# Kernel tuning notes

Hardware: AMD Instinct MI355X
Metric: run time of the kernel (lower is better)

Reference implementation:

```python
import jax, jax.numpy as jnp
import numpy as np

# dims: B batch, R seq_num (MSA rows), L seq_len (residues), D emb_dim, C n_emb_2D, H heads
B, R, L, D, C, H = 1, 256, 384, 512, 256, 4
HD = D // H
SCALE = np.float32((HD ** -0.5) / np.sqrt(L))  # head-dim scaling * seqlen_scaling (1/sqrt(L))
EPS = 1e-5


def setup_inputs() -> dict:
    key = jax.random.key(0)
    ks = jax.random.split(key, 6)
    s = 0.02
    return {
        "x": jax.random.normal(ks[0], (B, R, L, D), jnp.float32),
        "pair_feat": jax.random.normal(ks[1], (B, L, L, C), jnp.float32),
        "attn_mask": jnp.ones((B, L), jnp.int32),
        "ln_msa_g": jnp.ones((D,), jnp.float32),
        "ln_msa_b": jnp.zeros((D,), jnp.float32),
        "ln_pair_g": jnp.ones((C,), jnp.float32),
        "ln_pair_b": jnp.zeros((C,), jnp.float32),
        "W_pair": jax.random.normal(ks[2], (C, H), jnp.float32) * s,  # stacked per-head [C,1] linears
        "W_v": jax.random.normal(ks[3], (D, D), jnp.float32) * s,     # stacked per-head [D,HD] value proj
        "W_out": jax.random.normal(ks[4], (D, D), jnp.float32) * s,   # to_out (bias=False)
    }


def _ln(x, g, b):
    mu = jnp.mean(x, axis=-1, keepdims=True)
    var = jnp.mean(jnp.square(x - mu), axis=-1, keepdims=True)
    return (x - mu) * jax.lax.rsqrt(var + EPS) * g + b


def reference(x, pair_feat, attn_mask, ln_msa_g, ln_msa_b, ln_pair_g, ln_pair_b, W_pair, W_v, W_out):
    # MHPair_to_MSA.forward (eval mode, dropout=0)
    msa = _ln(x, ln_msa_g, ln_msa_b)                                  # [B,R,L,D]
    pf = (pair_feat + jnp.swapaxes(pair_feat, 1, 2)) * 0.5            # symmetrize
    pf = _ln(pf, ln_pair_g, ln_pair_b)                                # [B,L,L,C]
    # pair-feature-derived attention logits (no QK^T)
    logits = jnp.einsum('bijc,ch->bhij', pf * SCALE, W_pair)          # [B,H,L,L]
    V = jnp.einsum('brld,de->brle', msa, W_v).reshape(B, R, L, H, HD) # [B,R,L,H,HD]
    mask2 = attn_mask[:, :, None] * attn_mask[:, None, :]             # [B,L,L]
    logits = jnp.where(mask2[:, None, :, :] == 0,
                       jnp.finfo(logits.dtype).min, logits)
    attn = jax.nn.softmax(logits, axis=-1)                            # [B,H,L,L]
    out = jnp.einsum('bhij,brjhd->brihd', attn, V).reshape(B, R, L, D)
    out = out @ W_out                                                 # to_out, bias=False
    return x + out                                                    # residual
```

## Files before the change

kernel.cpp:

```cpp
#include <hip/hip_runtime.h>

#define L_   384
#define D_   512
#define C_   256
#define H_   4
#define RR_  256
#define M1_  98304
#define LL2_ 147456
#define NPAIR_BLOCKS 18480
#define TILE_ELEMS (128 * 64)

typedef __bf16 bf16x8 __attribute__((ext_vector_type(8)));
typedef float f32x4 __attribute__((ext_vector_type(4)));

__device__ __forceinline__ unsigned short f2bf_bits(float f) {
  union { float f; unsigned u; } v; v.f = f;
  return (unsigned short)((v.u + 0x7fffu + ((v.u >> 16) & 1u)) >> 16);
}
__device__ __forceinline__ __bf16 f2bf(float f) {
  union { unsigned short s; __bf16 b; } o; o.s = f2bf_bits(f);
  return o.b;
}

__device__ __forceinline__ float wave_sum(float v) {
#pragma unroll
  for (int o = 32; o > 0; o >>= 1) v += __shfl_xor(v, o);
  return v;
}
__device__ __forceinline__ float wave_max(float v) {
#pragma unroll
  for (int o = 32; o > 0; o >>= 1) v = fmaxf(v, __shfl_xor(v, o));
  return v;
}

__global__ __launch_bounds__(256) void ln_msa_kernel(
    const float* __restrict__ x, const float* __restrict__ g,
    const float* __restrict__ b, __bf16* __restrict__ msa) {
  int row = blockIdx.x * 4 + (threadIdx.x >> 6);
  int lane = threadIdx.x & 63;
  const float4* xr = (const float4*)(x + (size_t)row * D_ + lane * 8);
  float4 v0 = xr[0], v1 = xr[1];
  float s1 = v0.x + v0.y + v0.z + v0.w + v1.x + v1.y + v1.z + v1.w;
  float s2 = v0.x * v0.x + v0.y * v0.y + v0.z * v0.z + v0.w * v0.w +
             v1.x * v1.x + v1.y * v1.y + v1.z * v1.z + v1.w * v1.w;
#pragma unroll
  for (int o = 32; o > 0; o >>= 1) {
    s1 += __shfl_xor(s1, o);
    s2 += __shfl_xor(s2, o);
  }
  float mu = s1 * (1.0f / D_);
  float var = s2 * (1.0f / D_) - mu * mu;
  float rs = rsqrtf(var + 1e-5f);
  const float4* gp = (const float4*)(g + lane * 8);
  const float4* bp = (const float4*)(b + lane * 8);
  float4 g0 = gp[0], g1 = gp[1], b0 = bp[0], b1 = bp[1];
  float y[8];
  y[0] = (v0.x - mu) * rs * g0.x + b0.x;
  y[1] = (v0.y - mu) * rs * g0.y + b0.y;
  y[2] = (v0.z - mu) * rs * g0.z + b0.z;
  y[3] = (v0.w - mu) * rs * g0.w + b0.w;
  y[4] = (v1.x - mu) * rs * g1.x + b1.x;
  y[5] = (v1.y - mu) * rs * g1.y + b1.y;
  y[6] = (v1.z - mu) * rs * g1.z + b1.z;
  y[7] = (v1.w - mu) * rs * g1.w + b1.w;
  uint4 pk;
  pk.x = ((unsigned)f2bf_bits(y[1]) << 16) | f2bf_bits(y[0]);
  pk.y = ((unsigned)f2bf_bits(y[3]) << 16) | f2bf_bits(y[2]);
  pk.z = ((unsigned)f2bf_bits(y[5]) << 16) | f2bf_bits(y[4]);
  pk.w = ((unsigned)f2bf_bits(y[7]) << 16) | f2bf_bits(y[6]);
  *(uint4*)(msa + (size_t)row * D_ + lane * 8) = pk;
}

__global__ __launch_bounds__(256) void pair_logits_kernel(
    const float* __restrict__ pf, const int* __restrict__ mask,
    const float* __restrict__ g, const float* __restrict__ b,
    const float* __restrict__ Wp, float* __restrict__ logits) {
  unsigned wid = blockIdx.x * 4 + (threadIdx.x >> 6);
  int lane = threadIdx.x & 63;
  unsigned a = wid / 385u;
  unsigned c = wid - a * 385u;
  int i, j;
  if (c < 384u - a) { i = a; j = a + c; }
  else { i = 383 - a; j = i + (c - (384 - a)); }

  int c0 = lane * 4;
  float4 p1 = *(const float4*)(pf + ((size_t)i * L_ + j) * C_ + c0);
  float4 p2 = *(const float4*)(pf + ((size_t)j * L_ + i) * C_ + c0);
  float4 v;
  v.x = 0.5f * (p1.x + p2.x); v.y = 0.5f * (p1.y + p2.y);
  v.z = 0.5f * (p1.z + p2.z); v.w = 0.5f * (p1.w + p2.w);
  float s1 = v.x + v.y + v.z + v.w;
  float s2 = v.x * v.x + v.y * v.y + v.z * v.z + v.w * v.w;
#pragma unroll
  for (int o = 32; o > 0; o >>= 1) {
    s1 += __shfl_xor(s1, o);
    s2 += __shfl_xor(s2, o);
  }
  float mu = s1 * (1.0f / C_);
  float var = s2 * (1.0f / C_) - mu * mu;
  float rs = rsqrtf(var + 1e-5f);
  float4 gv = *(const float4*)(g + c0);
  float4 bv = *(const float4*)(b + c0);
  float y0 = (v.x - mu) * rs * gv.x + bv.x;
  float y1 = (v.y - mu) * rs * gv.y + bv.y;
  float y2 = (v.z - mu) * rs * gv.z + bv.z;
  float y3 = (v.w - mu) * rs * gv.w + bv.w;
  const float4* wp = (const float4*)Wp;
  float4 w0 = wp[c0], w1 = wp[c0 + 1], w2 = wp[c0 + 2], w3 = wp[c0 + 3];
  float4 t;
  t.x = y0 * w0.x + y1 * w1.x + y2 * w2.x + y3 * w3.x;
  t.y = y0 * w0.y + y1 * w1.y + y2 * w2.y + y3 * w3.y;
  t.z = y0 * w0.z + y1 * w1.z + y2 * w2.z + y3 * w3.z;
  t.w = y0 * w0.w + y1 * w1.w + y2 * w2.w + y3 * w3.w;
#pragma unroll
  for (int o = 32; o > 0; o >>= 1) {
    t.x += __shfl_xor(t.x, o);
    t.y += __shfl_xor(t.y, o);
    t.z += __shfl_xor(t.z, o);
    t.w += __shfl_xor(t.w, o);
  }
  if (lane < 8) {
    int h = lane & 3;
    int ii = (lane < 4) ? i : j;
    int jj = (lane < 4) ? j : i;
    bool ok = (mask[i] != 0) && (mask[j] != 0);
    const float NEG = -3.402823466e38f;
    const float SCALE = (float)(0.08838834764831845 / 19.595917942265423);
    float th = (h == 0) ? t.x : (h == 1) ? t.y : (h == 2) ? t.z : t.w;
    logits[(size_t)h * LL2_ + (size_t)ii * L_ + jj] = ok ? SCALE * th : NEG;
  }
}

__global__ __launch_bounds__(256) void softmax_kernel(
    const float* __restrict__ logits, __bf16* __restrict__ attn) {
  int wave = threadIdx.x >> 6, lane = threadIdx.x & 63;
  int row = blockIdx.x * 4 + wave;
  const float* lr = logits + (size_t)row * L_;
  float v[6];
#pragma unroll
  for (int t = 0; t < 6; ++t) v[t] = lr[lane + t * 64];
  float mx = v[0];
#pragma unroll
  for (int t = 1; t < 6; ++t) mx = fmaxf(mx, v[t]);
  mx = wave_max(mx);
  float s = 0.f;
#pragma unroll
  for (int t = 0; t < 6; ++t) { v[t] = __expf(v[t] - mx); s += v[t]; }
  s = wave_sum(s);
  float inv = 1.0f / s;
  __bf16* ar = attn + (size_t)row * L_;
#pragma unroll
  for (int t = 0; t < 6; ++t) ar[lane + t * 64] = f2bf(v[t] * inv);
}

__global__ __launch_bounds__(256) void wtrans_kernel(
    const float* __restrict__ Wv, const float* __restrict__ Wo,
    __bf16* __restrict__ WvT, __bf16* __restrict__ WoT) {
  int id = blockIdx.x * 256 + threadIdx.x;
  int m = id >> 18;
  int e = (id >> 9) & 511, d = id & 511;
  const float* W = m ? Wo : Wv;
  __bf16* T = m ? WoT : WvT;
  T[(size_t)e * 512 + d] = f2bf(W[(size_t)d * 512 + e]);
}

__device__ __forceinline__ void gload16(const void* g, void* l) {
  __builtin_amdgcn_global_load_lds(
      (const __attribute__((address_space(1))) void*)g,
      (__attribute__((address_space(3))) void*)l, 16, 0, 0);
}

__device__ __forceinline__ void stage_tile_async(__bf16* s, const __bf16* g, size_t ld) {
  int tid = threadIdx.x;
#pragma unroll
  for (int it = 0; it < 4; ++it) {
    int cid = it * 256 + tid;
    int row = cid >> 3, chk = cid & 7;
    int src_off = (chk * 16) ^ ((row & 7) << 4);
    gload16(g + (size_t)row * ld + (src_off >> 1), (char*)s + cid * 16);
  }
}

__device__ __forceinline__ bf16x8 frag_ld(const __bf16* s, int row, int k) {
  int sb = row * 128 + ((k * 2) ^ ((row & 7) << 4));
  return *(const bf16x8*)((const char*)s + sb);
}

__device__ __forceinline__ void gemm_mainloop(
    const __bf16* __restrict__ Arow, size_t ldA,
    const __bf16* __restrict__ Brow, size_t ldB,
    int K, __bf16* As, __bf16* Bs, f32x4 acc[4][4]) {
  int lane = threadIdx.x & 63, wave = threadIdx.x >> 6;
  int wm = (wave >> 1) * 64, wn = (wave & 1) * 64;
  int fr = lane & 15, fk = (lane >> 4) * 8;
  int nt = K >> 6;
  stage_tile_async(As, Arow, ldA);
  stage_tile_async(Bs, Brow, ldB);
  stage_tile_async(As + TILE_ELEMS, Arow + 64, ldA);
  stage_tile_async(Bs + TILE_ELEMS, Brow + 64, ldB);
  int cur = 0;
  for (int t = 0; t < nt; ++t) {
    if (t + 1 < nt) asm volatile("s_waitcnt vmcnt(8)" ::: "memory");
    else            asm volatile("s_waitcnt vmcnt(0)" ::: "memory");
    __builtin_amdgcn_s_barrier();
    __builtin_amdgcn_sched_barrier(0);
    const __bf16* Ab = As + cur * TILE_ELEMS;
    const __bf16* Bb = Bs + cur * TILE_ELEMS;
#pragma unroll
    for (int kk = 0; kk < 2; ++kk) {
      bf16x8 af[4], bfv[4];
#pragma unroll
      for (int mi = 0; mi < 4; ++mi) af[mi] = frag_ld(Ab, wm + mi * 16 + fr, kk * 32 + fk);
#pragma unroll
      for (int ni = 0; ni < 4; ++ni) bfv[ni] = frag_ld(Bb, wn + ni * 16 + fr, kk * 32 + fk);
#pragma unroll
      for (int mi = 0; mi < 4; ++mi)
#pragma unroll
        for (int ni = 0; ni < 4; ++ni)
          acc[mi][ni] = __builtin_amdgcn_mfma_f32_16x16x32_bf16(af[mi], bfv[ni], acc[mi][ni], 0, 0, 0);
    }
    __builtin_amdgcn_sched_barrier(0);
    __builtin_amdgcn_s_barrier();
    if (t + 2 < nt) {
      stage_tile_async(As + cur * TILE_ELEMS, Arow + (size_t)(t + 2) * 64, ldA);
      stage_tile_async(Bs + cur * TILE_ELEMS, Brow + (size_t)(t + 2) * 64, ldB);
    }
    cur ^= 1;
  }
}

__device__ __forceinline__ unsigned xcd_swz_3072(unsigned bid) {
  return (bid & 7u) * 384u + (bid >> 3);
}

__global__ __launch_bounds__(256) void gemm_vt_kernel(
    const __bf16* __restrict__ WvT, const __bf16* __restrict__ msa,
    __bf16* __restrict__ VT) {
  __shared__ __bf16 As[2 * TILE_ELEMS], Bs[2 * TILE_ELEMS];
  unsigned swz = xcd_swz_3072(blockIdx.x + 4 * blockIdx.y);
  int m0 = (swz & 3) * 128;
  int n0 = (swz >> 2) * 128;
  f32x4 acc[4][4] = {};
  gemm_mainloop(WvT + (size_t)m0 * D_, D_, msa + (size_t)n0 * D_, D_, D_, As, Bs, acc);
  int lane = threadIdx.x & 63, wave = threadIdx.x >> 6;
  int wm = (wave >> 1) * 64, wn = (wave & 1) * 64;
  int cr = (lane >> 4) * 4, cc = lane & 15;
#pragma unroll
  for (int mi = 0; mi < 4; ++mi)
#pragma unroll
    for (int ni = 0; ni < 4; ++ni)
#pragma unroll
      for (int rr = 0; rr < 4; ++rr) {
        int row = m0 + wm + mi * 16 + cr + rr;
        int col = n0 + wn + ni * 16 + cc;
        VT[(size_t)row * M1_ + col] = f2bf(acc[mi][ni][rr]);
      }
}

__global__ __launch_bounds__(256) void attnv_kernel(
    const __bf16* __restrict__ attn, const __bf16* __restrict__ VT,
    __bf16* __restrict__ out2) {
  __shared__ __bf16 As[2 * TILE_ELEMS], Bs[2 * TILE_ELEMS];
  unsigned swz = xcd_swz_3072(blockIdx.x + 3 * blockIdx.y);
  int it = swz % 3u;
  int rh = swz / 3u;
  int h = rh & 3, r = rh >> 2;
  const __bf16* A = attn + (size_t)h * LL2_ + (size_t)it * 128 * L_;
  const __bf16* Bt = VT + (size_t)(h * 128) * M1_ + (size_t)r * L_;
  f32x4 acc[4][4] = {};
  gemm_mainloop(A, L_, Bt, M1_, L_, As, Bs, acc);
  int lane = threadIdx.x & 63, wave = threadIdx.x >> 6;
  int wm = (wave >> 1) * 64, wn = (wave & 1) * 64;
  int cr = (lane >> 4) * 4, cc = lane & 15;
#pragma unroll
  for (int mi = 0; mi < 4; ++mi)
#pragma unroll
    for (int ni = 0; ni < 4; ++ni)
#pragma unroll
      for (int rr = 0; rr < 4; ++rr) {
        int row_i = it * 128 + wm + mi * 16 + cr + rr;
        int col = h * 128 + wn + ni * 16 + cc;
        out2[((size_t)r * L_ + row_i) * D_ + col] = f2bf(acc[mi][ni][rr]);
      }
}

__global__ __launch_bounds__(256) void gemm_out_kernel(
    const __bf16* __restrict__ out2, const __bf16* __restrict__ WoT,
    const float* __restrict__ x, float* __restrict__ out) {
  __shared__ __bf16 As[2 * TILE_ELEMS], Bs[2 * TILE_ELEMS];
  unsigned swz = xcd_swz_3072(blockIdx.x + 4 * blockIdx.y);
  int n0 = (swz & 3) * 128;
  int m0 = (swz >> 2) * 128;
  f32x4 acc[4][4] = {};
  gemm_mainloop(out2 + (size_t)m0 * D_, D_, WoT + (size_t)n0 * D_, D_, D_, As, Bs, acc);
  int lane = threadIdx.x & 63, wave = threadIdx.x >> 6;
  int wm = (wave >> 1) * 64, wn = (wave & 1) * 64;
  int cr = (lane >> 4) * 4, cc = lane & 15;
#pragma unroll
  for (int mi = 0; mi < 4; ++mi)
#pragma unroll
    for (int ni = 0; ni < 4; ++ni)
#pragma unroll
      for (int rr = 0; rr < 4; ++rr) {
        int row = m0 + wm + mi * 16 + cr + rr;
        int col = n0 + wn + ni * 16 + cc;
        size_t idx = (size_t)row * D_ + col;
        out[idx] = x[idx] + acc[mi][ni][rr];
      }
}

extern "C" void kernel_launch(void* const* d_in, const int* in_sizes, int n_in,
                              void* d_out, int out_size, void* d_ws, size_t ws_size,
                              hipStream_t stream) {
  const float* x      = (const float*)d_in[0];
  const float* pair   = (const float*)d_in[1];
  const int*   mask   = (const int*)d_in[2];
  const float* g_msa  = (const float*)d_in[3];
  const float* b_msa  = (const float*)d_in[4];
  const float* g_pair = (const float*)d_in[5];
  const float* b_pair = (const float*)d_in[6];
  const float* Wp     = (const float*)d_in[7];
  const float* Wv     = (const float*)d_in[8];
  const float* Wo     = (const float*)d_in[9];
  float* out = (float*)d_out;

  char* p = (char*)d_ws;
  auto alloc = [&](size_t bytes) {
    char* r = p;
    p += (bytes + 255) & ~(size_t)255;
    return r;
  };
  __bf16* msa    = (__bf16*)alloc((size_t)M1_ * D_ * 2);
  __bf16* VT     = (__bf16*)alloc((size_t)D_ * M1_ * 2);
  float*  logits = (float*)alloc((size_t)H_ * LL2_ * 4);
  __bf16* attn   = (__bf16*)alloc((size_t)H_ * LL2_ * 2);
  __bf16* WvT    = (__bf16*)alloc((size_t)512 * 512 * 2);
  __bf16* WoT    = (__bf16*)alloc((size_t)512 * 512 * 2);
  __bf16* out2   = msa;

  wtrans_kernel<<<2048, 256, 0, stream>>>(Wv, Wo, WvT, WoT);
  ln_msa_kernel<<<M1_ / 4, 256, 0, stream>>>(x, g_msa, b_msa, msa);
  gemm_vt_kernel<<<dim3(4, M1_ / 128), 256, 0, stream>>>(WvT, msa, VT);
  pair_logits_kernel<<<NPAIR_BLOCKS, 256, 0, stream>>>(pair, mask, g_pair, b_pair, Wp, logits);
  softmax_kernel<<<(H_ * L_) / 4, 256, 0, stream>>>(logits, attn);
  attnv_kernel<<<dim3(3, RR_ * H_), 256, 0, stream>>>(attn, VT, out2);
  gemm_out_kernel<<<dim3(4, M1_ / 128), 256, 0, stream>>>(out2, WoT, x, out);
}
```

Measured before the change: 388.1 us.

## Use 256x256 tiles with 512-thread blocks for the V and output GEMMs

Replaces the 128x128 tiled GEMM mainloop in the V-projection and output-projection kernels with a 256x256 tile computed by 8 waves, each owning a 128x64 sub-tile. The aim is to raise arithmetic intensity and halve how often each operand is reloaded from global memory. It also sets wave priority around the MFMA bursts and adjusts the XCD swizzle for the smaller grid. In exchange it uses more LDS and registers per block (one block per CU) and launches fewer blocks, which may reduce latency hiding.

```diff
diff --git a/kernel.cpp b/kernel.cpp
--- a/kernel.cpp
+++ b/kernel.cpp
@@ -9,6 +9,7 @@
 #define LL2_ 147456
 #define NPAIR_BLOCKS 18480
 #define TILE_ELEMS (128 * 64)
+#define TILE256_ELEMS (256 * 64)
 
 typedef __bf16 bf16x8 __attribute__((ext_vector_type(8)));
 typedef float f32x4 __attribute__((ext_vector_type(4)));
@@ -181,6 +182,17 @@
   }
 }
 
+__device__ __forceinline__ void stage_tile256(__bf16* s, const __bf16* g, size_t ld) {
+  int tid = threadIdx.x;
+#pragma unroll
+  for (int it = 0; it < 4; ++it) {
+    int cid = it * 512 + tid;
+    int row = cid >> 3, chk = cid & 7;
+    int src_off = (chk * 16) ^ ((row & 7) << 4);
+    gload16(g + (size_t)row * ld + (src_off >> 1), (char*)s + cid * 16);
+  }
+}
+
 __device__ __forceinline__ bf16x8 frag_ld(const __bf16* s, int row, int k) {
   int sb = row * 128 + ((k * 2) ^ ((row & 7) << 4));
   return *(const bf16x8*)((const char*)s + sb);
@@ -229,24 +241,72 @@
   }
 }
 
+__device__ __forceinline__ void gemm_mainloop256(
+    const __bf16* __restrict__ Arow, size_t ldA,
+    const __bf16* __restrict__ Brow, size_t ldB,
+    int K, __bf16* As, __bf16* Bs, f32x4 acc[8][4]) {
+  int lane = threadIdx.x & 63, wave = threadIdx.x >> 6;
+  int wm = (wave >> 2) * 128, wn = (wave & 3) * 64;
+  int fr = lane & 15, fk = (lane >> 4) * 8;
+  int nt = K >> 6;
+  stage_tile256(As, Arow, ldA);
+  stage_tile256(Bs, Brow, ldB);
+  stage_tile256(As + TILE256_ELEMS, Arow + 64, ldA);
+  stage_tile256(Bs + TILE256_ELEMS, Brow + 64, ldB);
+  int cur = 0;
+  for (int t = 0; t < nt; ++t) {
+    if (t + 1 < nt) asm volatile("s_waitcnt vmcnt(8)" ::: "memory");
+    else            asm volatile("s_waitcnt vmcnt(0)" ::: "memory");
+    __builtin_amdgcn_s_barrier();
+    __builtin_amdgcn_sched_barrier(0);
+    const __bf16* Ab = As + cur * TILE256_ELEMS;
+    const __bf16* Bb = Bs + cur * TILE256_ELEMS;
+#pragma unroll
+    for (int kk = 0; kk < 2; ++kk) {
+      bf16x8 af[8], bfv[4];
+#pragma unroll
+      for (int mi = 0; mi < 8; ++mi) af[mi] = frag_ld(Ab, wm + mi * 16 + fr, kk * 32 + fk);
+#pragma unroll
+      for (int ni = 0; ni < 4; ++ni) bfv[ni] = frag_ld(Bb, wn + ni * 16 + fr, kk * 32 + fk);
+      __builtin_amdgcn_s_setprio(1);
+#pragma unroll
+      for (int mi = 0; mi < 8; ++mi)
+#pragma unroll
+        for (int ni = 0; ni < 4; ++ni)
+          acc[mi][ni] = __builtin_amdgcn_mfma_f32_16x16x32_bf16(af[mi], bfv[ni], acc[mi][ni], 0, 0, 0);
+      __builtin_amdgcn_s_setprio(0);
+    }
+    __builtin_amdgcn_sched_barrier(0);
+    __builtin_amdgcn_s_barrier();
+    if (t + 2 < nt) {
+      stage_tile256(As + cur * TILE256_ELEMS, Arow + (size_t)(t + 2) * 64, ldA);
+      stage_tile256(Bs + cur * TILE256_ELEMS, Brow + (size_t)(t + 2) * 64, ldB);
+    }
+    cur ^= 1;
+  }
+}
+
 __device__ __forceinline__ unsigned xcd_swz_3072(unsigned bid) {
   return (bid & 7u) * 384u + (bid >> 3);
 }
-
-__global__ __launch_bounds__(256) void gemm_vt_kernel(
+__device__ __forceinline__ unsigned xcd_swz_768(unsigned bid) {
+  return (bid & 7u) * 96u + (bid >> 3);
+}
+
+__global__ __launch_bounds__(512, 1) void gemm_vt_kernel(
     const __bf16* __restrict__ WvT, const __bf16* __restrict__ msa,
     __bf16* __restrict__ VT) {
-  __shared__ __bf16 As[2 * TILE_ELEMS], Bs[2 * TILE_ELEMS];
-  unsigned swz = xcd_swz_3072(blockIdx.x + 4 * blockIdx.y);
-  int m0 = (swz & 3) * 128;
-  int n0 = (swz >> 2) * 128;
-  f32x4 acc[4][4] = {};
-  gemm_mainloop(WvT + (size_t)m0 * D_, D_, msa + (size_t)n0 * D_, D_, D_, As, Bs, acc);
+  __shared__ __bf16 As[2 * TILE256_ELEMS], Bs[2 * TILE256_ELEMS];
+  unsigned swz = xcd_swz_768(blockIdx.x + 2 * blockIdx.y);
+  int m0 = (swz & 1) * 256;
+  int n0 = (swz >> 1) * 256;
+  f32x4 acc[8][4] = {};
+  gemm_mainloop256(WvT + (size_t)m0 * D_, D_, msa + (size_t)n0 * D_, D_, D_, As, Bs, acc);
   int lane = threadIdx.x & 63, wave = threadIdx.x >> 6;
-  int wm = (wave >> 1) * 64, wn = (wave & 1) * 64;
+  int wm = (wave >> 2) * 128, wn = (wave & 3) * 64;
   int cr = (lane >> 4) * 4, cc = lane & 15;
 #pragma unroll
-  for (int mi = 0; mi < 4; ++mi)
+  for (int mi = 0; mi < 8; ++mi)
 #pragma unroll
     for (int ni = 0; ni < 4; ++ni)
 #pragma unroll
@@ -284,20 +344,20 @@
       }
 }
 
-__global__ __launch_bounds__(256) void gemm_out_kernel(
+__global__ __launch_bounds__(512, 1) void gemm_out_kernel(
     const __bf16* __restrict__ out2, const __bf16* __restrict__ WoT,
     const float* __restrict__ x, float* __restrict__ out) {
-  __shared__ __bf16 As[2 * TILE_ELEMS], Bs[2 * TILE_ELEMS];
-  unsigned swz = xcd_swz_3072(blockIdx.x + 4 * blockIdx.y);
-  int n0 = (swz & 3) * 128;
-  int m0 = (swz >> 2) * 128;
-  f32x4 acc[4][4] = {};
-  gemm_mainloop(out2 + (size_t)m0 * D_, D_, WoT + (size_t)n0 * D_, D_, D_, As, Bs, acc);
+  __shared__ __bf16 As[2 * TILE256_ELEMS], Bs[2 * TILE256_ELEMS];
+  unsigned swz = xcd_swz_768(blockIdx.x + 2 * blockIdx.y);
+  int n0 = (swz & 1) * 256;
+  int m0 = (swz >> 1) * 256;
+  f32x4 acc[8][4] = {};
+  gemm_mainloop256(out2 + (size_t)m0 * D_, D_, WoT + (size_t)n0 * D_, D_, D_, As, Bs, acc);
   int lane = threadIdx.x & 63, wave = threadIdx.x >> 6;
-  int wm = (wave >> 1) * 64, wn = (wave & 1) * 64;
+  int wm = (wave >> 2) * 128, wn = (wave & 3) * 64;
   int cr = (lane >> 4) * 4, cc = lane & 15;
 #pragma unroll
-  for (int mi = 0; mi < 4; ++mi)
+  for (int mi = 0; mi < 8; ++mi)
 #pragma unroll
     for (int ni = 0; ni < 4; ++ni)
 #pragma unroll
@@ -340,9 +400,9 @@
 
   wtrans_kernel<<<2048, 256, 0, stream>>>(Wv, Wo, WvT, WoT);
   ln_msa_kernel<<<M1_ / 4, 256, 0, stream>>>(x, g_msa, b_msa, msa);
-  gemm_vt_kernel<<<dim3(4, M1_ / 128), 256, 0, stream>>>(WvT, msa, VT);
+  gemm_vt_kernel<<<dim3(2, M1_ / 256), 512, 0, stream>>>(WvT, msa, VT);
   pair_logits_kernel<<<NPAIR_BLOCKS, 256, 0, stream>>>(pair, mask, g_pair, b_pair, Wp, logits);
   softmax_kernel<<<(H_ * L_) / 4, 256, 0, stream>>>(logits, attn);
   attnv_kernel<<<dim3(3, RR_ * H_), 256, 0, stream>>>(attn, VT, out2);
-  gemm_out_kernel<<<dim3(4, M1_ / 128), 256, 0, stream>>>(out2, WoT, x, out);
-}
+  gemm_out_kernel<<<dim3(2, M1_ / 256), 512, 0, stream>>>(out2, WoT, x, out);
+}
```

New measurement: 375.7 us. 1.03x faster.
